# Kernel optimization log

Hardware: AMD Instinct MI355X
Metric: run time of the kernel (lower is better)

The kernel has to match this reference:

```python
import jax, jax.numpy as jnp
import numpy as np

B, S, E, H = 2, 2048, 1024, 16
HD = E // H


def setup_inputs() -> dict:
    key = jax.random.key(0)
    ks = jax.random.split(key, 9)
    s = 1.0 / np.sqrt(E)
    return {
        "x": jax.random.normal(ks[0], (B, S, E), dtype=jnp.float32),
        "wq": jax.random.uniform(ks[1], (E, E), jnp.float32, -s, s),
        "bq": jax.random.uniform(ks[2], (E,), jnp.float32, -s, s),
        "wk": jax.random.uniform(ks[3], (E, E), jnp.float32, -s, s),
        "bk": jax.random.uniform(ks[4], (E,), jnp.float32, -s, s),
        "wv": jax.random.uniform(ks[5], (E, E), jnp.float32, -s, s),
        "bv": jax.random.uniform(ks[6], (E,), jnp.float32, -s, s),
        "wo": jax.random.uniform(ks[7], (E, E), jnp.float32, -s, s),
        "bo": jax.random.uniform(ks[8], (E,), jnp.float32, -s, s),
    }


def reference(x, wq, bq, wk, bk, wv, bv, wo, bo):
    b, s, e = x.shape
    # QKV projections, reshape to [b, h, s, hd]
    def proj(w, bias):
        y = jnp.einsum('bse,ef->bsf', x, w.T) + bias
        return y.reshape(b, s, H, HD).transpose(0, 2, 1, 3)
    q = proj(wq, bq)
    k = proj(wk, bk)
    v = proj(wv, bv)
    score = jnp.einsum('bhqd,bhkd->bhqk', q, k) / jnp.sqrt(jnp.float32(HD))
    # original: exp(x)/sum(exp(x)) + 1e-8  == softmax(x) + 1e-8
    attn = jax.nn.softmax(score, axis=-1) + 1e-8
    out = jnp.einsum('bhqk,bhkd->bhqd', attn, v)
    out = out.transpose(0, 2, 1, 3).reshape(b, s, e)
    return jnp.einsum('bse,ef->bsf', out, wo.T) + bo
```

## Files before the change

### kernel.cpp

```cpp
#include <hip/hip_runtime.h>
#include <hip/hip_bf16.h>
#include <cstdint>

#define SS 2048
#define EE 1024
#define HH 16
#define HDD 64

typedef __attribute__((ext_vector_type(8))) __bf16 bf16x8;
typedef __attribute__((ext_vector_type(4))) float f32x4;

#define MFMA16(a, b, c) __builtin_amdgcn_mfma_f32_16x16x32_bf16((a), (b), (c), 0, 0, 0)

__device__ __forceinline__ unsigned short f2bf(float f) {
    unsigned int u = __builtin_bit_cast(unsigned int, f);
    u += 0x7FFFu + ((u >> 16) & 1u);
    return (unsigned short)(u >> 16);
}

__device__ __forceinline__ void gll16(const unsigned short* g, unsigned short* l) {
    __builtin_amdgcn_global_load_lds(
        (__attribute__((address_space(1))) unsigned int*)g,
        (__attribute__((address_space(3))) unsigned int*)l, 16, 0, 0);
}

__global__ __launch_bounds__(256) void cvt_all(
    const float* __restrict__ x, const float* __restrict__ wq, const float* __restrict__ wk,
    const float* __restrict__ wv, const float* __restrict__ wo,
    unsigned short* __restrict__ xb, unsigned short* __restrict__ wqb, unsigned short* __restrict__ wkb,
    unsigned short* __restrict__ wvb, unsigned short* __restrict__ wob) {
    int idx = blockIdx.x * 256 + threadIdx.x;
    int i4 = idx << 2;
    const float* src;
    unsigned short* dst;
    int off;
    if (i4 < 4194304) { src = x; dst = xb; off = i4; }
    else {
        int w = (i4 - 4194304) >> 20;
        off = (i4 - 4194304) & 1048575;
        if (w == 0) { src = wq; dst = wqb; }
        else if (w == 1) { src = wk; dst = wkb; }
        else if (w == 2) { src = wv; dst = wvb; }
        else { src = wo; dst = wob; }
    }
    float4 v = *(const float4*)&src[off];
    unsigned int p0 = (unsigned int)f2bf(v.x) | ((unsigned int)f2bf(v.y) << 16);
    unsigned int p1 = (unsigned int)f2bf(v.z) | ((unsigned int)f2bf(v.w) << 16);
    uint2 u; u.x = p0; u.y = p1;
    *(uint2*)&dst[off] = u;
}

template <int MODE, int BMT, int BNT>
__device__ __forceinline__ void gemm_core(
    unsigned short* __restrict__ lsA,
    unsigned short* __restrict__ lsB,
    const unsigned short* __restrict__ A, const unsigned short* __restrict__ W,
    const float* __restrict__ bias, void* __restrict__ out, int bm, int bn) {
    constexpr int IT = BMT / 32, JT = BNT / 32;
    constexpr int ASTR = BMT * 32, BSTR = BNT * 32;
    const int t = threadIdx.x;
    const int lane = t & 63, l15 = lane & 15, quad = lane >> 4;
    const int wave = t >> 6;
    const int wm = (wave >> 1) * (BMT / 2), wn = (wave & 1) * (BNT / 2);

    const int cg = ((t & 3) ^ ((t >> 3) & 3)) * 8;
    const unsigned short* ga = A + (size_t)(bm + (t >> 2)) * 1024 + cg;
    const unsigned short* gb = W + (size_t)(bn + (t >> 2)) * 1024 + cg;

    f32x4 acc[IT][JT];
    for (int i = 0; i < IT; i++)
        for (int j = 0; j < JT; j++) acc[i][j] = (f32x4){0.f, 0.f, 0.f, 0.f};

    const int swz = (l15 >> 1) & 3;

    gll16(ga, &lsA[t * 8]);
    if (BMT == 128) gll16(ga + 64 * 1024, &lsA[2048 + t * 8]);
    gll16(gb, &lsB[t * 8]);
    if (BNT == 128) gll16(gb + 64 * 1024, &lsB[2048 + t * 8]);

    for (int it = 0; it < 32; it++) {
        const int cur = it & 1, nxt = cur ^ 1;
        __syncthreads();

        if (it < 31) {
            const int k0 = (it + 1) * 32;
            gll16(ga + k0, &lsA[nxt * ASTR + t * 8]);
            if (BMT == 128) gll16(ga + k0 + 64 * 1024, &lsA[nxt * ASTR + 2048 + t * 8]);
            gll16(gb + k0, &lsB[nxt * BSTR + t * 8]);
            if (BNT == 128) gll16(gb + k0 + 64 * 1024, &lsB[nxt * BSTR + 2048 + t * 8]);
        }

        bf16x8 af[IT], bfr[JT];
        for (int i = 0; i < IT; i++)
            af[i] = *(const bf16x8*)&lsA[cur * ASTR + (wm + i * 16 + l15) * 32 + ((quad ^ swz) * 8)];
        for (int j = 0; j < JT; j++)
            bfr[j] = *(const bf16x8*)&lsB[cur * BSTR + (wn + j * 16 + l15) * 32 + ((quad ^ swz) * 8)];
        for (int i = 0; i < IT; i++)
            for (int j = 0; j < JT; j++) acc[i][j] = MFMA16(af[i], bfr[j], acc[i][j]);
    }

    for (int j = 0; j < JT; j++) {
        int n = bn + wn + j * 16 + l15;
        float bj = bias[n];
        for (int i = 0; i < IT; i++) {
            int m0 = bm + wm + i * 16 + quad * 4;
            int srow0 = m0 & 2047, bidx = m0 >> 11;
            if (MODE == 3) {
                size_t headb = ((size_t)bidx * HH + (n >> 6)) * (SS * HDD);
                size_t base = headb + (size_t)(srow0 >> 6) * 4096 +
                              (size_t)(((srow0 >> 4) & 3) * 8 + ((n & 63) >> 3)) * 128 + (n & 7);
                for (int rg = 0; rg < 4; rg++)
                    ((unsigned short*)out)[base + (size_t)((srow0 & 15) + rg) * 8] = f2bf(acc[i][j][rg] + bj);
            } else if (MODE == 4) {
                size_t headb = ((size_t)bidx * HH + (n >> 6)) * (SS * HDD);
                size_t addr = headb + (size_t)(srow0 >> 6) * 4096 + (size_t)((n & 63) >> 4) * 1024 +
                              (size_t)(((srow0 >> 5) & 1) * 4 + ((srow0 >> 3) & 3)) * 128 +
                              (size_t)(n & 15) * 8 + (srow0 & 7);
                float v0 = acc[i][j][0] + bj, v1 = acc[i][j][1] + bj;
                float v2 = acc[i][j][2] + bj, v3 = acc[i][j][3] + bj;
                uint2 w;
                w.x = (unsigned int)f2bf(v0) | ((unsigned int)f2bf(v1) << 16);
                w.y = (unsigned int)f2bf(v2) | ((unsigned int)f2bf(v3) << 16);
                *(uint2*)&((unsigned short*)out)[addr] = w;
            } else {
                for (int rg = 0; rg < 4; rg++) {
                    float val = acc[i][j][rg] + bj;
                    int m = m0 + rg;
                    if (MODE == 0) {
                        ((unsigned short*)out)[(((size_t)(m >> 11) * HH + (n >> 6)) * SS + (m & 2047)) * HDD + (n & 63)] = f2bf(val);
                    } else {
                        ((float*)out)[(size_t)m * 1024 + n] = val;
                    }
                }
            }
        }
    }
}

__global__ __launch_bounds__(256, 4) void gemm_qkv(
    const unsigned short* __restrict__ xb,
    const unsigned short* __restrict__ wqb, const unsigned short* __restrict__ wkb,
    const unsigned short* __restrict__ wvb,
    const float* __restrict__ bq, const float* __restrict__ bk, const float* __restrict__ bv,
    unsigned short* qb, unsigned short* kb, unsigned short* vtb) {
    __shared__ unsigned short shA[2 * 4096];
    __shared__ unsigned short shB[2 * 2048];
    const int blk = blockIdx.x;
    const int u = blk & 7, r = blk >> 3;
    const int by = u + 8 * (r & 3);
    const int rest = r >> 2;
    const int bx = rest & 15;
    const int z = rest >> 4;
    if (z == 0)      gemm_core<0, 128, 64>(shA, shB, xb, wqb, bq, qb,  by * 128, bx * 64);
    else if (z == 1) gemm_core<3, 128, 64>(shA, shB, xb, wkb, bk, kb,  by * 128, bx * 64);
    else             gemm_core<4, 128, 64>(shA, shB, xb, wvb, bv, vtb, by * 128, bx * 64);
}

__global__ __launch_bounds__(256, 4) void gemm_out(
    const unsigned short* __restrict__ ob, const unsigned short* __restrict__ wob,
    const float* __restrict__ bo, float* __restrict__ out) {
    __shared__ unsigned short shA[2 * 2048];
    __shared__ unsigned short shB[2 * 2048];
    const int blk = blockIdx.x;
    const int u = blk & 7, r = blk >> 3;
    const int by = u + 8 * (r & 7);
    const int bx = r >> 3;
    gemm_core<1, 64, 64>(shA, shB, ob, wob, bo, out, by * 64, bx * 64);
}

#define PSTR 72

__global__ __launch_bounds__(256) void attn_fwd(
    const unsigned short* __restrict__ qb, const unsigned short* __restrict__ kb,
    const unsigned short* __restrict__ vtb, unsigned short* __restrict__ ob) {
    __shared__ unsigned short lsK[2][4096];
    __shared__ unsigned short lsV[2][4096];
    __shared__ unsigned short lsP[4 * 32 * PSTR];
    const int t = threadIdx.x, lane = t & 63, l15 = lane & 15, quad = lane >> 4, wave = t >> 6;
    const int blk = blockIdx.x;
    const int u = blk & 7, r = blk >> 3;
    const int bh = u + 8 * (r & 3);
    const int qt = r >> 2;
    const size_t hoff = (size_t)bh * (SS * HDD);
    const float C = 0.125f * 1.44269504088896f;

    bf16x8 qf[2][2];
    const int qrow = qt * 128 + wave * 32;
    for (int i = 0; i < 2; i++)
        for (int ks = 0; ks < 2; ks++) {
            bf16x8 raw = *(const bf16x8*)&qb[hoff + (size_t)(qrow + i * 16 + l15) * HDD + ks * 32 + quad * 8];
            unsigned short tmp[8];
            *(bf16x8*)tmp = raw;
            for (int j = 0; j < 8; j++) {
                float f = __builtin_bit_cast(float, (unsigned int)tmp[j] << 16);
                tmp[j] = f2bf(f * C);
            }
            qf[i][ks] = *(const bf16x8*)tmp;
        }

    unsigned short onesbuf[8];
    for (int j = 0; j < 8; j++) onesbuf[j] = 0x3F80;
    const bf16x8 onesf = *(const bf16x8*)onesbuf;

    f32x4 lacc[2];
    f32x4 o[2][4];
    for (int i = 0; i < 2; i++) {
        lacc[i] = (f32x4){0.f, 0.f, 0.f, 0.f};
        for (int jh = 0; jh < 4; jh++) o[i][jh] = (f32x4){0.f, 0.f, 0.f, 0.f};
    }

    const unsigned short* gk = kb + hoff;
    const unsigned short* gv = vtb + hoff;
    const int pbase = wave * 32 * PSTR;
    const int foff = quad * 128 + l15 * 8;

    gll16(gk + t * 8, &lsK[0][t * 8]);
    gll16(gk + 2048 + t * 8, &lsK[0][2048 + t * 8]);
    gll16(gv + t * 8, &lsV[0][t * 8]);
    gll16(gv + 2048 + t * 8, &lsV[0][2048 + t * 8]);

    for (int kt = 0; kt < 32; kt++) {
        const int cur = kt & 1, nxt = cur ^ 1;
        __syncthreads();

        if (kt < 31) {
            const unsigned short* gkn = gk + (kt + 1) * 4096;
            const unsigned short* gvn = gv + (kt + 1) * 4096;
            gll16(gkn + t * 8, &lsK[nxt][t * 8]);
            gll16(gkn + 2048 + t * 8, &lsK[nxt][2048 + t * 8]);
            gll16(gvn + t * 8, &lsV[nxt][t * 8]);
            gll16(gvn + 2048 + t * 8, &lsV[nxt][2048 + t * 8]);
        }

        bf16x8 kfr[4][2];
        for (int j = 0; j < 4; j++)
            for (int ks = 0; ks < 2; ks++)
                kfr[j][ks] = *(const bf16x8*)&lsK[cur][j * 1024 + ks * 512 + foff];

        f32x4 st[4][2];
        for (int j = 0; j < 4; j++)
            for (int i = 0; i < 2; i++) {
                f32x4 z = (f32x4){0.f, 0.f, 0.f, 0.f};
                z = MFMA16(kfr[j][0], qf[i][0], z);
                z = MFMA16(kfr[j][1], qf[i][1], z);
                st[j][i] = z;
            }

        for (int j = 0; j < 4; j++)
            for (int i = 0; i < 2; i++) {
                float e0 = __builtin_amdgcn_exp2f(st[j][i][0]);
                float e1 = __builtin_amdgcn_exp2f(st[j][i][1]);
                float e2 = __builtin_amdgcn_exp2f(st[j][i][2]);
                float e3 = __builtin_amdgcn_exp2f(st[j][i][3]);
                uint2 w;
                w.x = (__builtin_bit_cast(unsigned int, e0) >> 16) |
                      (__builtin_bit_cast(unsigned int, e1) & 0xFFFF0000u);
                w.y = (__builtin_bit_cast(unsigned int, e2) >> 16) |
                      (__builtin_bit_cast(unsigned int, e3) & 0xFFFF0000u);
                *(uint2*)&lsP[pbase + (i * 16 + l15) * PSTR + j * 16 + quad * 4] = w;
            }

        bf16x8 pf[2][2], vf[4][2];
        for (int i = 0; i < 2; i++)
            for (int ks = 0; ks < 2; ks++)
                pf[i][ks] = *(const bf16x8*)&lsP[pbase + (i * 16 + l15) * PSTR + ks * 32 + quad * 8];
        for (int jh = 0; jh < 4; jh++)
            for (int ks = 0; ks < 2; ks++)
                vf[jh][ks] = *(const bf16x8*)&lsV[cur][jh * 1024 + ks * 512 + foff];
        for (int i = 0; i < 2; i++) {
            for (int jh = 0; jh < 4; jh++) {
                o[i][jh] = MFMA16(pf[i][0], vf[jh][0], o[i][jh]);
                o[i][jh] = MFMA16(pf[i][1], vf[jh][1], o[i][jh]);
            }
            lacc[i] = MFMA16(pf[i][0], onesf, lacc[i]);
            lacc[i] = MFMA16(pf[i][1], onesf, lacc[i]);
        }
    }

    const int b = bh >> 4, h = bh & 15;
    for (int i = 0; i < 2; i++)
        for (int rg = 0; rg < 4; rg++) {
            float inv = 1.f / lacc[i][rg];
            int srow = qt * 128 + wave * 32 + i * 16 + quad * 4 + rg;
            size_t rowoff = ((size_t)b * SS + srow) * EE + h * 64;
            for (int jh = 0; jh < 4; jh++)
                ob[rowoff + jh * 16 + l15] = f2bf(o[i][jh][rg] * inv);
        }
}

extern "C" void kernel_launch(void* const* d_in, const int* in_sizes, int n_in,
                              void* d_out, int out_size, void* d_ws, size_t ws_size,
                              hipStream_t stream) {
    const float* x  = (const float*)d_in[0];
    const float* wq = (const float*)d_in[1];
    const float* bq = (const float*)d_in[2];
    const float* wk = (const float*)d_in[3];
    const float* bk = (const float*)d_in[4];
    const float* wv = (const float*)d_in[5];
    const float* bv = (const float*)d_in[6];
    const float* wo = (const float*)d_in[7];
    const float* bo = (const float*)d_in[8];

    char* ws = (char*)d_ws;
    unsigned short* xb  = (unsigned short*)(ws + 0);
    unsigned short* wqb = (unsigned short*)(ws + 8388608);
    unsigned short* wkb = (unsigned short*)(ws + 10485760);
    unsigned short* wvb = (unsigned short*)(ws + 12582912);
    unsigned short* wob = (unsigned short*)(ws + 14680064);
    unsigned short* qb  = (unsigned short*)(ws + 16777216);
    unsigned short* kb  = (unsigned short*)(ws + 25165824);
    unsigned short* vtb = (unsigned short*)(ws + 33554432);
    unsigned short* ob  = xb;

    cvt_all<<<8192, 256, 0, stream>>>(x, wq, wk, wv, wo, xb, wqb, wkb, wvb, wob);
    gemm_qkv<<<1536, 256, 0, stream>>>(xb, wqb, wkb, wvb, bq, bk, bv, qb, kb, vtb);
    attn_fwd<<<512, 256, 0, stream>>>(qb, kb, vtb, ob);
    gemm_out<<<1024, 256, 0, stream>>>(ob, wob, bo, (float*)d_out);
}
```

Before: 207.1 us.

## Split attention KV loop across two wave groups and enlarge GEMM tiles

```diff
diff --git a/kernel.cpp b/kernel.cpp
--- a/kernel.cpp
+++ b/kernel.cpp
@@ -137,46 +137,50 @@
     }
 }
 
-__global__ __launch_bounds__(256, 4) void gemm_qkv(
+__global__ __launch_bounds__(256) void gemm_qkv(
     const unsigned short* __restrict__ xb,
     const unsigned short* __restrict__ wqb, const unsigned short* __restrict__ wkb,
     const unsigned short* __restrict__ wvb,
     const float* __restrict__ bq, const float* __restrict__ bk, const float* __restrict__ bv,
     unsigned short* qb, unsigned short* kb, unsigned short* vtb) {
     __shared__ unsigned short shA[2 * 4096];
+    __shared__ unsigned short shB[2 * 4096];
+    const int blk = blockIdx.x;
+    const int u = blk & 7, r = blk >> 3;
+    const int by = u + 8 * (r & 3);
+    const int rest = r >> 2;
+    const int bx = rest & 7, z = rest >> 3;
+    if (z == 0)      gemm_core<0, 128, 128>(shA, shB, xb, wqb, bq, qb,  by * 128, bx * 128);
+    else if (z == 1) gemm_core<3, 128, 128>(shA, shB, xb, wkb, bk, kb,  by * 128, bx * 128);
+    else             gemm_core<4, 128, 128>(shA, shB, xb, wvb, bv, vtb, by * 128, bx * 128);
+}
+
+__global__ __launch_bounds__(256) void gemm_out(
+    const unsigned short* __restrict__ ob, const unsigned short* __restrict__ wob,
+    const float* __restrict__ bo, float* __restrict__ out) {
+    __shared__ unsigned short shA[2 * 4096];
     __shared__ unsigned short shB[2 * 2048];
     const int blk = blockIdx.x;
     const int u = blk & 7, r = blk >> 3;
     const int by = u + 8 * (r & 3);
-    const int rest = r >> 2;
-    const int bx = rest & 15;
-    const int z = rest >> 4;
-    if (z == 0)      gemm_core<0, 128, 64>(shA, shB, xb, wqb, bq, qb,  by * 128, bx * 64);
-    else if (z == 1) gemm_core<3, 128, 64>(shA, shB, xb, wkb, bk, kb,  by * 128, bx * 64);
-    else             gemm_core<4, 128, 64>(shA, shB, xb, wvb, bv, vtb, by * 128, bx * 64);
-}
-
-__global__ __launch_bounds__(256, 4) void gemm_out(
-    const unsigned short* __restrict__ ob, const unsigned short* __restrict__ wob,
-    const float* __restrict__ bo, float* __restrict__ out) {
-    __shared__ unsigned short shA[2 * 2048];
-    __shared__ unsigned short shB[2 * 2048];
-    const int blk = blockIdx.x;
-    const int u = blk & 7, r = blk >> 3;
-    const int by = u + 8 * (r & 7);
-    const int bx = r >> 3;
-    gemm_core<1, 64, 64>(shA, shB, ob, wob, bo, out, by * 64, bx * 64);
+    const int bx = r >> 2;
+    gemm_core<1, 128, 64>(shA, shB, ob, wob, bo, out, by * 128, bx * 64);
 }
 
 #define PSTR 72
 
-__global__ __launch_bounds__(256) void attn_fwd(
+__global__ __launch_bounds__(512, 4) void attn_fwd(
     const unsigned short* __restrict__ qb, const unsigned short* __restrict__ kb,
     const unsigned short* __restrict__ vtb, unsigned short* __restrict__ ob) {
-    __shared__ unsigned short lsK[2][4096];
-    __shared__ unsigned short lsV[2][4096];
-    __shared__ unsigned short lsP[4 * 32 * PSTR];
-    const int t = threadIdx.x, lane = t & 63, l15 = lane & 15, quad = lane >> 4, wave = t >> 6;
+    __shared__ unsigned short sh[8192 + 8192 + 8 * 32 * PSTR];
+    unsigned short* lsK = sh;
+    unsigned short* lsV = sh + 8192;
+    unsigned short* lsP = sh + 16384;
+    const int t = threadIdx.x, lane = t & 63, l15 = lane & 15, quad = lane >> 4;
+    const int wave = t >> 6;
+    const int half = wave >> 2;
+    const int wq = wave & 3;
+    const int tg = t & 255;
     const int blk = blockIdx.x;
     const int u = blk & 7, r = blk >> 3;
     const int bh = u + 8 * (r & 3);
@@ -185,7 +189,7 @@
     const float C = 0.125f * 1.44269504088896f;
 
     bf16x8 qf[2][2];
-    const int qrow = qt * 128 + wave * 32;
+    const int qrow = qt * 128 + wq * 32;
     for (int i = 0; i < 2; i++)
         for (int ks = 0; ks < 2; ks++) {
             bf16x8 raw = *(const bf16x8*)&qb[hoff + (size_t)(qrow + i * 16 + l15) * HDD + ks * 32 + quad * 8];
@@ -209,33 +213,25 @@
         for (int jh = 0; jh < 4; jh++) o[i][jh] = (f32x4){0.f, 0.f, 0.f, 0.f};
     }
 
-    const unsigned short* gk = kb + hoff;
-    const unsigned short* gv = vtb + hoff;
+    const unsigned short* gk = kb + hoff + (size_t)half * 16 * 4096;
+    const unsigned short* gv = vtb + hoff + (size_t)half * 16 * 4096;
+    unsigned short* myK = lsK + half * 4096;
+    unsigned short* myV = lsV + half * 4096;
     const int pbase = wave * 32 * PSTR;
     const int foff = quad * 128 + l15 * 8;
 
-    gll16(gk + t * 8, &lsK[0][t * 8]);
-    gll16(gk + 2048 + t * 8, &lsK[0][2048 + t * 8]);
-    gll16(gv + t * 8, &lsV[0][t * 8]);
-    gll16(gv + 2048 + t * 8, &lsV[0][2048 + t * 8]);
-
-    for (int kt = 0; kt < 32; kt++) {
-        const int cur = kt & 1, nxt = cur ^ 1;
+    gll16(gk + tg * 8, myK + tg * 8);
+    gll16(gk + 2048 + tg * 8, myK + 2048 + tg * 8);
+    gll16(gv + tg * 8, myV + tg * 8);
+    gll16(gv + 2048 + tg * 8, myV + 2048 + tg * 8);
+
+    for (int kt = 0; kt < 16; kt++) {
         __syncthreads();
-
-        if (kt < 31) {
-            const unsigned short* gkn = gk + (kt + 1) * 4096;
-            const unsigned short* gvn = gv + (kt + 1) * 4096;
-            gll16(gkn + t * 8, &lsK[nxt][t * 8]);
-            gll16(gkn + 2048 + t * 8, &lsK[nxt][2048 + t * 8]);
-            gll16(gvn + t * 8, &lsV[nxt][t * 8]);
-            gll16(gvn + 2048 + t * 8, &lsV[nxt][2048 + t * 8]);
-        }
 
         bf16x8 kfr[4][2];
         for (int j = 0; j < 4; j++)
             for (int ks = 0; ks < 2; ks++)
-                kfr[j][ks] = *(const bf16x8*)&lsK[cur][j * 1024 + ks * 512 + foff];
+                kfr[j][ks] = *(const bf16x8*)&myK[j * 1024 + ks * 512 + foff];
 
         f32x4 st[4][2];
         for (int j = 0; j < 4; j++)
@@ -266,7 +262,7 @@
                 pf[i][ks] = *(const bf16x8*)&lsP[pbase + (i * 16 + l15) * PSTR + ks * 32 + quad * 8];
         for (int jh = 0; jh < 4; jh++)
             for (int ks = 0; ks < 2; ks++)
-                vf[jh][ks] = *(const bf16x8*)&lsV[cur][jh * 1024 + ks * 512 + foff];
+                vf[jh][ks] = *(const bf16x8*)&myV[jh * 1024 + ks * 512 + foff];
         for (int i = 0; i < 2; i++) {
             for (int jh = 0; jh < 4; jh++) {
                 o[i][jh] = MFMA16(pf[i][0], vf[jh][0], o[i][jh]);
@@ -275,17 +271,45 @@
             lacc[i] = MFMA16(pf[i][0], onesf, lacc[i]);
             lacc[i] = MFMA16(pf[i][1], onesf, lacc[i]);
         }
-    }
-
-    const int b = bh >> 4, h = bh & 15;
-    for (int i = 0; i < 2; i++)
-        for (int rg = 0; rg < 4; rg++) {
-            float inv = 1.f / lacc[i][rg];
-            int srow = qt * 128 + wave * 32 + i * 16 + quad * 4 + rg;
-            size_t rowoff = ((size_t)b * SS + srow) * EE + h * 64;
+
+        if (kt < 15) {
+            __syncthreads();
+            const unsigned short* gkn = gk + (kt + 1) * 4096;
+            const unsigned short* gvn = gv + (kt + 1) * 4096;
+            gll16(gkn + tg * 8, myK + tg * 8);
+            gll16(gkn + 2048 + tg * 8, myK + 2048 + tg * 8);
+            gll16(gvn + tg * 8, myV + tg * 8);
+            gll16(gvn + 2048 + tg * 8, myV + 2048 + tg * 8);
+        }
+    }
+
+    __syncthreads();
+    float* cb = (float*)sh;
+    float* lb = cb + 8192;
+    const int lslot = wq * 64 + lane;
+    if (half == 1) {
+        for (int i = 0; i < 2; i++)
             for (int jh = 0; jh < 4; jh++)
-                ob[rowoff + jh * 16 + l15] = f2bf(o[i][jh][rg] * inv);
-        }
+                for (int rg = 0; rg < 4; rg++)
+                    cb[(i * 16 + jh * 4 + rg) * 256 + lslot] = o[i][jh][rg];
+        for (int i = 0; i < 2; i++)
+            for (int rg = 0; rg < 4; rg++)
+                lb[(i * 4 + rg) * 256 + lslot] = lacc[i][rg];
+    }
+    __syncthreads();
+    if (half == 0) {
+        const int b = bh >> 4, h = bh & 15;
+        for (int i = 0; i < 2; i++)
+            for (int rg = 0; rg < 4; rg++) {
+                float inv = 1.f / (lacc[i][rg] + lb[(i * 4 + rg) * 256 + lslot]);
+                int srow = qrow + i * 16 + quad * 4 + rg;
+                size_t rowoff = ((size_t)b * SS + srow) * EE + h * 64;
+                for (int jh = 0; jh < 4; jh++) {
+                    float val = o[i][jh][rg] + cb[(i * 16 + jh * 4 + rg) * 256 + lslot];
+                    ob[rowoff + jh * 16 + l15] = f2bf(val * inv);
+                }
+            }
+    }
 }
 
 extern "C" void kernel_launch(void* const* d_in, const int* in_sizes, int n_in,
@@ -313,7 +337,7 @@
     unsigned short* ob  = xb;
 
     cvt_all<<<8192, 256, 0, stream>>>(x, wq, wk, wv, wo, xb, wqb, wkb, wvb, wob);
-    gemm_qkv<<<1536, 256, 0, stream>>>(xb, wqb, wkb, wvb, bq, bk, bv, qb, kb, vtb);
-    attn_fwd<<<512, 256, 0, stream>>>(qb, kb, vtb, ob);
-    gemm_out<<<1024, 256, 0, stream>>>(ob, wob, bo, (float*)d_out);
-}
+    gemm_qkv<<<768, 256, 0, stream>>>(xb, wqb, wkb, wvb, bq, bk, bv, qb, kb, vtb);
+    attn_fwd<<<512, 512, 0, stream>>>(qb, kb, vtb, ob);
+    gemm_out<<<512, 256, 0, stream>>>(ob, wob, bo, (float*)d_out);
+}
```

New measurement: 190.5 us. 1.09x faster.
